# Performance work log

Hardware: AMD Instinct MI355X
Metric: run time of the kernel (lower is better)

## Reference

```python
import jax, jax.numpy as jnp
import numpy as np

N = 50000
E_RAND = 800000
IN0 = 128
HEADS = 4
C = 64  # per-head out channels
HC = HEADS * C  # 256, concat output width
SLOPE = 0.2
DIMS_IN = [IN0, HC, HC]


def _gat_layer(x, src, dst, W, att_src, att_dst, bias):
    # x: [N, F_in]; W: [F_in, H*C]; att_*: [H, C]; bias: [H*C]
    h = (x @ W).reshape(N, HEADS, C)                      # [N,H,C]
    a_src = jnp.einsum('nhc,hc->nh', h, att_src)          # [N,H]
    a_dst = jnp.einsum('nhc,hc->nh', h, att_dst)          # [N,H]
    e = jax.nn.leaky_relu(a_src[src] + a_dst[dst], SLOPE)  # [E,H]
    # segment softmax over incoming edges per destination node
    m = jax.ops.segment_max(e, dst, num_segments=N)       # [N,H]
    m = jnp.where(jnp.isfinite(m), m, 0.0)
    ex = jnp.exp(e - m[dst])                              # [E,H]
    denom = jax.ops.segment_sum(ex, dst, num_segments=N)  # [N,H]
    alpha = ex / (denom[dst] + 1e-16)                     # [E,H]
    msg = h[src] * alpha[:, :, None]                      # [E,H,C]
    out = jax.ops.segment_sum(msg, dst, num_segments=N)   # [N,H,C]
    return out.reshape(N, HC) + bias


def setup_inputs() -> dict:
    key = jax.random.key(0)
    ks = jax.random.split(key, 16)
    x = jax.random.normal(ks[0], (N, IN0), dtype=jnp.float32)
    src = jax.random.randint(ks[1], (E_RAND,), 0, N, dtype=jnp.int32)
    dst = jax.random.randint(ks[2], (E_RAND,), 0, N, dtype=jnp.int32)
    loops = jnp.arange(N, dtype=jnp.int32)  # PyG GATConv adds self-loops
    edge_index = jnp.stack([jnp.concatenate([src, loops]),
                            jnp.concatenate([dst, loops])])  # [2, E_RAND+N]
    inp = {'x': x, 'edge_index': edge_index}
    ki = 3
    for l, f_in in enumerate(DIMS_IN):
        s = 1.0 / np.sqrt(f_in)
        inp[f'W{l}'] = jax.random.uniform(ks[ki], (f_in, HC), jnp.float32, -s, s)
        inp[f'att_src{l}'] = jax.random.uniform(ks[ki + 1], (HEADS, C), jnp.float32, -s, s)
        inp[f'att_dst{l}'] = jax.random.uniform(ks[ki + 2], (HEADS, C), jnp.float32, -s, s)
        inp[f'bias{l}'] = jnp.zeros((HC,), jnp.float32)
        ki += 3
    return inp


def reference(x, edge_index, W0, att_src0, att_dst0, bias0,
              W1, att_src1, att_dst1, bias1,
              W2, att_src2, att_dst2, bias2):
    src, dst = edge_index[0], edge_index[1]
    params = [(W0, att_src0, att_dst0, bias0),
              (W1, att_src1, att_dst1, bias1),
              (W2, att_src2, att_dst2, bias2)]
    for W, a_s, a_d, b in params:
        x = jax.nn.relu(_gat_layer(x, src, dst, W, a_s, a_d, b))
    return x
```

## Files before the change

kernel.cpp:

```cpp
#include <hip/hip_runtime.h>
#include <hip/hip_fp16.h>
#include <math.h>

#define IN0    128
#define HEADS  4
#define CDIM   64
#define HC     256
#define SLOPE  0.2f
#define NPAD   50176
#define BK     32

typedef __attribute__((ext_vector_type(8))) _Float16 f16x8;
typedef __attribute__((ext_vector_type(4))) float f32x4;

__device__ __forceinline__ float h2f(ushort u) {
    __half h = *(const __half*)&u;
    return __half2float(h);
}
__device__ __forceinline__ ushort f2h(float f) {
    __half h = __float2half_rn(f);
    return *(ushort*)&h;
}


__device__ __forceinline__ void wconv_body(const float* __restrict__ W,
                                           ushort* __restrict__ Wc, int K, int b) {
    int tid = b * 256 + threadIdx.x;
    int n = tid & 255;
    int k = tid >> 8;
    if (k >= K) return;
    Wc[(size_t)(k >> 5) * (HC * BK) + n * BK + (k & 31)] = f2h(W[(size_t)k * HC + n]);
}

__global__ __launch_bounds__(256) void k_prep(
        const int* __restrict__ dst_rand, int E_rand, int* __restrict__ deg,
        const float* __restrict__ x0, ushort* __restrict__ Xc, int totalx,
        const float* __restrict__ W0, ushort* __restrict__ Wc0,
        const float* __restrict__ W1, ushort* __restrict__ Wc1,
        const float* __restrict__ W2, ushort* __restrict__ Wc2,
        int B0, int B1) {
    int b = blockIdx.x;
    if (b < B0) {
        int i = b * 256 + threadIdx.x;
        if (i < E_rand) atomicAdd(&deg[dst_rand[i]], 1);
        return;
    }
    b -= B0;
    if (b < B1) {
        int i = b * 256 + threadIdx.x;
        if (i < totalx) {
            int n = i >> 7, k = i & 127;
            Xc[(size_t)(k >> 5) * (NPAD * BK) + n * BK + (k & 31)] = f2h(x0[i]);
        }
        return;
    }
    b -= B1;
    if (b < 128) { wconv_body(W0, Wc0, 128, b); return; }
    b -= 128;
    if (b < 256) { wconv_body(W1, Wc1, 256, b); return; }
    b -= 256;
    wconv_body(W2, Wc2, 256, b);
}


__global__ __launch_bounds__(1024) void k_scan(const int* __restrict__ deg, int Nn,
                                               int* __restrict__ rowptr,
                                               int* __restrict__ cur) {
    __shared__ int smem[1024];
    int tid = threadIdx.x;
    int pre = 0;
    int limit = blockIdx.x * 1024;
    for (int i = tid; i < limit; i += 1024) pre += deg[i];
    smem[tid] = pre;
    __syncthreads();
    #pragma unroll
    for (int d = 512; d >= 1; d >>= 1) {
        if (tid < d) smem[tid] += smem[tid + d];
        __syncthreads();
    }
    int s_off = smem[0];
    __syncthreads();
    int i = blockIdx.x * 1024 + tid;
    int v = (i < Nn) ? deg[i] : 0;
    smem[tid] = v;
    __syncthreads();
    #pragma unroll
    for (int d = 1; d < 1024; d <<= 1) {
        int t = 0;
        if (tid >= d) t = smem[tid - d];
        __syncthreads();
        smem[tid] += t;
        __syncthreads();
    }
    if (i < Nn) {
        int e = s_off + smem[tid] - v;
        rowptr[i] = e;
        cur[i] = e;
    }
    if (blockIdx.x == gridDim.x - 1 && tid == 1023) rowptr[Nn] = s_off + smem[1023];
}

__global__ void k_scatter(const int* __restrict__ src, const int* __restrict__ dst, int E_rand,
                          int* __restrict__ cur, int* __restrict__ csr_src) {
    int i = blockIdx.x * blockDim.x + threadIdx.x;
    if (i < E_rand) {
        int d = dst[i];
        int p = atomicAdd(&cur[d], 1);
        csr_src[p] = src[i];
    }
}


template<int K>
__global__ __launch_bounds__(256) void k_gemm_att(const ushort* __restrict__ Xc,
                                                  const ushort* __restrict__ Wc,
                                                  const float* __restrict__ attS,
                                                  const float* __restrict__ attD,
                                                  ushort* __restrict__ H16out,
                                                  float* __restrict__ a_src_v,
                                                  float* __restrict__ a_dst_v,
                                                  int M) {
    int id    = blockIdx.x;
    int group = id >> 4;
    int sub   = id & 15;
    int row0  = (group * 8 + (sub & 7)) * 128;
    int colb  = sub >> 3;
    int col0  = colb * 128;

    int t    = threadIdx.x;
    int wave = t >> 6, lane = t & 63;
    int wm = wave & 1, wn = wave >> 1;
    int quad = lane >> 4, l16 = lane & 15;

    f32x4 acc[4][4];
    #pragma unroll
    for (int i = 0; i < 4; i++)
        #pragma unroll
        for (int j = 0; j < 4; j++) acc[i][j] = (f32x4){0.f, 0.f, 0.f, 0.f};

    constexpr int NK = K / BK;
    #pragma unroll
    for (int kc = 0; kc < NK; kc++) {
        f16x8 a[4], b[4];
        #pragma unroll
        for (int mt = 0; mt < 4; mt++) {
            size_t ga = (size_t)kc * (NPAD * BK)
                      + (size_t)(row0 + wm * 64 + mt * 16 + l16) * BK + quad * 8;
            a[mt] = *(const f16x8*)&Xc[ga];
        }
        #pragma unroll
        for (int nt = 0; nt < 4; nt++) {
            size_t gb = (size_t)kc * (HC * BK)
                      + (size_t)(col0 + wn * 64 + nt * 16 + l16) * BK + quad * 8;
            b[nt] = *(const f16x8*)&Wc[gb];
        }
        #pragma unroll
        for (int mt = 0; mt < 4; mt++)
            #pragma unroll
            for (int nt = 0; nt < 4; nt++)
                acc[mt][nt] = __builtin_amdgcn_mfma_f32_16x16x32_f16(a[mt], b[nt], acc[mt][nt], 0, 0, 0);
    }

    #pragma unroll
    for (int mt = 0; mt < 4; mt++) {
        #pragma unroll
        for (int r = 0; r < 4; r++) {
            int row = row0 + wm*64 + mt*16 + quad*4 + r;
            if (row >= M) continue;
            #pragma unroll
            for (int nt = 0; nt < 4; nt++) {
                size_t idx = (size_t)row * HC + col0 + wn*64 + nt*16 + l16;
                H16out[idx] = f2h(acc[mt][nt][r]);
            }
        }
    }

    int headw = colb * 2 + wn;
    float sS[4], sD[4];
    #pragma unroll
    for (int nt = 0; nt < 4; nt++) {
        sS[nt] = attS[headw * CDIM + nt*16 + l16];
        sD[nt] = attD[headw * CDIM + nt*16 + l16];
    }
    #pragma unroll
    for (int mt = 0; mt < 4; mt++) {
        #pragma unroll
        for (int r = 0; r < 4; r++) {
            float ps = 0.f, pd = 0.f;
            #pragma unroll
            for (int nt = 0; nt < 4; nt++) {
                float av = acc[mt][nt][r];
                ps += av * sS[nt];
                pd += av * sD[nt];
            }
            #pragma unroll
            for (int d = 1; d <= 8; d <<= 1) {
                ps += __shfl_xor(ps, d);
                pd += __shfl_xor(pd, d);
            }
            int row = row0 + wm*64 + mt*16 + quad*4 + r;
            if (l16 == 0 && row < M) {
                a_src_v[row * HEADS + headw] = ps;
                a_dst_v[row * HEADS + headw] = pd;
            }
        }
    }
}


__global__ __launch_bounds__(256) void k_aggregate(
        const ushort* __restrict__ H16,
        const float* __restrict__ a_src_v, const float* __restrict__ a_dst_v,
        const int* __restrict__ rowptr, const int* __restrict__ csr_src,
        const float* __restrict__ bias,
        float* __restrict__ out_f32,
        ushort* __restrict__ out_h16c,
        int Nn) {
    int wave = threadIdx.x >> 6;
    int lane = threadIdx.x & 63;
    int n = blockIdx.x * 4 + wave;
    if (n >= Nn) return;

    int e16 = lane >> 2;
    int hs  = lane & 3;
    int ha  = lane >> 4;
    int c4  = (lane & 15) * 4;

    int beg = rowptr[n], end = rowptr[n + 1];
    int deg = end - beg;
    float adst_s = a_dst_v[n * HEADS + hs];
    float es = a_src_v[n * HEADS + hs] + adst_s;
    es = (es > 0.f) ? es : SLOPE * es;
    float ex_self_s = __expf(es);

    float ssum = 0.f;
    float4 acc = make_float4(0.f, 0.f, 0.f, 0.f);
    const char* Hb = (const char*)H16 + (ha * CDIM + c4) * 2;

    for (int base = 0; base < deg; base += 16) {
        int cnt = min(16, deg - base);
        int s_l = 0; float ex_l = 0.f;
        if (e16 < cnt) {
            s_l = csr_src[beg + base + e16];
            float e = a_src_v[s_l * HEADS + hs] + adst_s;
            e = (e > 0.f) ? e : SLOPE * e;
            ex_l = __expf(e);
            ssum += ex_l;
        }
        int off_l = s_l * (HC * 2);
        int cnt4 = (cnt + 3) & ~3;
        for (int j = 0; j < cnt4; j += 4) {
            float a0 = __shfl(ex_l,  (j + 0) * 4 + ha);
            int   o0 = __shfl(off_l, (j + 0) * 4 + ha);
            float a1 = __shfl(ex_l,  (j + 1) * 4 + ha);
            int   o1 = __shfl(off_l, (j + 1) * 4 + ha);
            float a2 = __shfl(ex_l,  (j + 2) * 4 + ha);
            int   o2 = __shfl(off_l, (j + 2) * 4 + ha);
            float a3 = __shfl(ex_l,  (j + 3) * 4 + ha);
            int   o3 = __shfl(off_l, (j + 3) * 4 + ha);
            ushort4 u0 = *(const ushort4*)(Hb + o0);
            ushort4 u1 = *(const ushort4*)(Hb + o1);
            ushort4 u2 = *(const ushort4*)(Hb + o2);
            ushort4 u3 = *(const ushort4*)(Hb + o3);
            acc.x += a0 * h2f(u0.x); acc.y += a0 * h2f(u0.y);
            acc.z += a0 * h2f(u0.z); acc.w += a0 * h2f(u0.w);
            acc.x += a1 * h2f(u1.x); acc.y += a1 * h2f(u1.y);
            acc.z += a1 * h2f(u1.z); acc.w += a1 * h2f(u1.w);
            acc.x += a2 * h2f(u2.x); acc.y += a2 * h2f(u2.y);
            acc.z += a2 * h2f(u2.z); acc.w += a2 * h2f(u2.w);
            acc.x += a3 * h2f(u3.x); acc.y += a3 * h2f(u3.y);
            acc.z += a3 * h2f(u3.z); acc.w += a3 * h2f(u3.w);
        }
    }
    #pragma unroll
    for (int d = 4; d <= 32; d <<= 1) ssum += __shfl_xor(ssum, d);
    ssum += ex_self_s;
    float den_a = __shfl(ssum, ha);
    float exs_a = __shfl(ex_self_s, ha);

    ushort4 us = *(const ushort4*)((const char*)H16 + (size_t)n * (HC * 2) + (ha * CDIM + c4) * 2);
    float rden = 1.f / (den_a + 1e-16f);
    float4 b = *(const float4*)&bias[ha * CDIM + c4];
    float4 o;
    o.x = fmaxf((acc.x + exs_a * h2f(us.x)) * rden + b.x, 0.f);
    o.y = fmaxf((acc.y + exs_a * h2f(us.y)) * rden + b.y, 0.f);
    o.z = fmaxf((acc.z + exs_a * h2f(us.z)) * rden + b.z, 0.f);
    o.w = fmaxf((acc.w + exs_a * h2f(us.w)) * rden + b.w, 0.f);

    if (out_f32) {
        *(float4*)&out_f32[(size_t)n * HC + ha * CDIM + c4] = o;
    }
    if (out_h16c) {
        int ch = ha * CDIM + c4;
        size_t idx = (size_t)(ch >> 5) * (NPAD * BK) + (size_t)n * BK + (ch & 31);
        *(ushort4*)&out_h16c[idx] = make_ushort4(f2h(o.x), f2h(o.y), f2h(o.z), f2h(o.w));
    }
}


extern "C" void kernel_launch(void* const* d_in, const int* in_sizes, int n_in,
                              void* d_out, int out_size, void* d_ws, size_t ws_size,
                              hipStream_t stream) {
    const float* x0   = (const float*)d_in[0];
    const int*   eidx = (const int*)d_in[1];
    int Nn = in_sizes[0] / IN0;
    int E  = in_sizes[1] / 2;
    int E_rand = E - Nn;
    const int* srcp = eidx;
    const int* dstp = eidx + E;

    const float* Wl[3]    = {(const float*)d_in[2],  (const float*)d_in[6],  (const float*)d_in[10]};
    const float* attS[3]  = {(const float*)d_in[3],  (const float*)d_in[7],  (const float*)d_in[11]};
    const float* attD[3]  = {(const float*)d_in[4],  (const float*)d_in[8],  (const float*)d_in[12]};
    const float* biasl[3] = {(const float*)d_in[5],  (const float*)d_in[9],  (const float*)d_in[13]};
    int Kdims[3] = {IN0, HC, HC};

    char* p = (char*)d_ws;
    ushort* h16    = (ushort*)p; p += (size_t)NPAD * HC * sizeof(ushort);
    ushort* Xc     = (ushort*)p; p += (size_t)NPAD * HC * sizeof(ushort);
    float*  a_src_v= (float*)p;  p += (size_t)Nn * HEADS * sizeof(float);
    float*  a_dst_v= (float*)p;  p += (size_t)Nn * HEADS * sizeof(float);
    int*    rowptr = (int*)p;    p += (size_t)(Nn + 1) * sizeof(int);
    int*    deg    = (int*)p;    p += (size_t)Nn * sizeof(int);
    int*    cur    = (int*)p;    p += (size_t)Nn * sizeof(int);
    int*    csr_src= (int*)p;    p += (size_t)E_rand * sizeof(int);
    ushort* Wc[3];
    for (int l = 0; l < 3; l++) {
        Wc[l] = (ushort*)p; p += (size_t)HC * Kdims[l] * sizeof(ushort);
    }

    int NB = (Nn + 1023) / 1024;
    int B0 = (E_rand + 255) / 256;
    int B1 = (Nn * IN0 + 255) / 256;
    int Bprep = B0 + B1 + 128 + 256 + 256;

    hipMemsetAsync(deg, 0, (size_t)Nn * sizeof(int), stream);
    k_prep<<<Bprep, 256, 0, stream>>>(dstp, E_rand, deg,
                                      x0, Xc, Nn * IN0,
                                      Wl[0], Wc[0], Wl[1], Wc[1], Wl[2], Wc[2],
                                      B0, B1);
    k_scan<<<NB, 1024, 0, stream>>>(deg, Nn, rowptr, cur);
    k_scatter<<<(E_rand + 255) / 256, 256, 0, stream>>>(srcp, dstp, E_rand, cur, csr_src);

    dim3 g(784);
    dim3 ga((Nn + 3) / 4);
    for (int l = 0; l < 3; l++) {
        if (l == 0)
            k_gemm_att<128><<<g, 256, 0, stream>>>(Xc, Wc[l], attS[l], attD[l],
                                                   h16, a_src_v, a_dst_v, Nn);
        else
            k_gemm_att<256><<<g, 256, 0, stream>>>(Xc, Wc[l], attS[l], attD[l],
                                                   h16, a_src_v, a_dst_v, Nn);
        if (l < 2) {
            k_aggregate<<<ga, 256, 0, stream>>>(h16, a_src_v, a_dst_v, rowptr, csr_src,
                                                biasl[l], nullptr, Xc, Nn);
        } else {
            k_aggregate<<<ga, 256, 0, stream>>>(h16, a_src_v, a_dst_v, rowptr, csr_src,
                                                biasl[l], (float*)d_out, nullptr, Nn);
        }
    }
}
```

Measured before the change: 383.3 us.

## Store H in channel-sliced layout and split aggregation into 8 column slices

The GEMM now writes H in a 32-channel-sliced column-major-block layout and stores attention logits head-major. Aggregation launches 8 blocks per node group, each handling one 32-channel slice, so gathered rows are contiguous 64-byte chunks and blockIdx ordering keeps each slice's working set in cache. This trades more redundant softmax/index work (computed once per slice) for smaller, more cache-local gathers and more parallelism.

```diff
diff --git a/kernel.cpp b/kernel.cpp
--- a/kernel.cpp
+++ b/kernel.cpp
@@ -169,7 +169,8 @@
             if (row >= M) continue;
             #pragma unroll
             for (int nt = 0; nt < 4; nt++) {
-                size_t idx = (size_t)row * HC + col0 + wn*64 + nt*16 + l16;
+                int col = col0 + wn*64 + nt*16 + l16;
+                size_t idx = (size_t)(col >> 5) * (NPAD * 32) + (size_t)row * 32 + (col & 31);
                 H16out[idx] = f2h(acc[mt][nt][r]);
             }
         }
@@ -200,8 +201,8 @@
             }
             int row = row0 + wm*64 + mt*16 + quad*4 + r;
             if (l16 == 0 && row < M) {
-                a_src_v[row * HEADS + headw] = ps;
-                a_dst_v[row * HEADS + headw] = pd;
+                a_src_v[(size_t)headw * M + row] = ps;
+                a_dst_v[(size_t)headw * M + row] = pd;
             }
         }
     }
@@ -209,91 +210,84 @@
 
 
 __global__ __launch_bounds__(256) void k_aggregate(
-        const ushort* __restrict__ H16,
-        const float* __restrict__ a_src_v, const float* __restrict__ a_dst_v,
+        const ushort* __restrict__ Hc,
+        const float* __restrict__ a_srcP,
+        const float* __restrict__ a_dstP,
         const int* __restrict__ rowptr, const int* __restrict__ csr_src,
         const float* __restrict__ bias,
         float* __restrict__ out_f32,
         ushort* __restrict__ out_h16c,
         int Nn) {
-    int wave = threadIdx.x >> 6;
-    int lane = threadIdx.x & 63;
-    int n = blockIdx.x * 4 + wave;
+    int lane  = threadIdx.x & 63;
+    int slice = blockIdx.x & 7;
+    int n = (blockIdx.x >> 3) * 4 + (threadIdx.x >> 6);
     if (n >= Nn) return;
-
-    int e16 = lane >> 2;
-    int hs  = lane & 3;
-    int ha  = lane >> 4;
-    int c4  = (lane & 15) * 4;
+    int h  = slice >> 1;
+    int es = lane >> 3;
+    int c8 = lane & 7;
+
+    const char* Hs = (const char*)(Hc + (size_t)slice * (NPAD * 32));
+    const float* aS = a_srcP + (size_t)h * Nn;
 
     int beg = rowptr[n], end = rowptr[n + 1];
     int deg = end - beg;
-    float adst_s = a_dst_v[n * HEADS + hs];
-    float es = a_src_v[n * HEADS + hs] + adst_s;
-    es = (es > 0.f) ? es : SLOPE * es;
-    float ex_self_s = __expf(es);
+    float adst = a_dstP[(size_t)h * Nn + n];
+    float e_self = aS[n] + adst;
+    e_self = (e_self > 0.f) ? e_self : SLOPE * e_self;
+    float ex_self = __expf(e_self);
 
     float ssum = 0.f;
     float4 acc = make_float4(0.f, 0.f, 0.f, 0.f);
-    const char* Hb = (const char*)H16 + (ha * CDIM + c4) * 2;
-
-    for (int base = 0; base < deg; base += 16) {
-        int cnt = min(16, deg - base);
+
+    for (int base = 0; base < deg; base += 64) {
+        int cnt = min(64, deg - base);
         int s_l = 0; float ex_l = 0.f;
-        if (e16 < cnt) {
-            s_l = csr_src[beg + base + e16];
-            float e = a_src_v[s_l * HEADS + hs] + adst_s;
+        if (lane < cnt) {
+            s_l = csr_src[beg + base + lane];
+            float e = aS[s_l] + adst;
             e = (e > 0.f) ? e : SLOPE * e;
             ex_l = __expf(e);
             ssum += ex_l;
         }
-        int off_l = s_l * (HC * 2);
-        int cnt4 = (cnt + 3) & ~3;
-        for (int j = 0; j < cnt4; j += 4) {
-            float a0 = __shfl(ex_l,  (j + 0) * 4 + ha);
-            int   o0 = __shfl(off_l, (j + 0) * 4 + ha);
-            float a1 = __shfl(ex_l,  (j + 1) * 4 + ha);
-            int   o1 = __shfl(off_l, (j + 1) * 4 + ha);
-            float a2 = __shfl(ex_l,  (j + 2) * 4 + ha);
-            int   o2 = __shfl(off_l, (j + 2) * 4 + ha);
-            float a3 = __shfl(ex_l,  (j + 3) * 4 + ha);
-            int   o3 = __shfl(off_l, (j + 3) * 4 + ha);
-            ushort4 u0 = *(const ushort4*)(Hb + o0);
-            ushort4 u1 = *(const ushort4*)(Hb + o1);
-            ushort4 u2 = *(const ushort4*)(Hb + o2);
-            ushort4 u3 = *(const ushort4*)(Hb + o3);
-            acc.x += a0 * h2f(u0.x); acc.y += a0 * h2f(u0.y);
-            acc.z += a0 * h2f(u0.z); acc.w += a0 * h2f(u0.w);
-            acc.x += a1 * h2f(u1.x); acc.y += a1 * h2f(u1.y);
-            acc.z += a1 * h2f(u1.z); acc.w += a1 * h2f(u1.w);
-            acc.x += a2 * h2f(u2.x); acc.y += a2 * h2f(u2.y);
-            acc.z += a2 * h2f(u2.z); acc.w += a2 * h2f(u2.w);
-            acc.x += a3 * h2f(u3.x); acc.y += a3 * h2f(u3.y);
-            acc.z += a3 * h2f(u3.z); acc.w += a3 * h2f(u3.w);
-        }
-    }
-    #pragma unroll
-    for (int d = 4; d <= 32; d <<= 1) ssum += __shfl_xor(ssum, d);
-    ssum += ex_self_s;
-    float den_a = __shfl(ssum, ha);
-    float exs_a = __shfl(ex_self_s, ha);
-
-    ushort4 us = *(const ushort4*)((const char*)H16 + (size_t)n * (HC * 2) + (ha * CDIM + c4) * 2);
-    float rden = 1.f / (den_a + 1e-16f);
-    float4 b = *(const float4*)&bias[ha * CDIM + c4];
-    float4 o;
-    o.x = fmaxf((acc.x + exs_a * h2f(us.x)) * rden + b.x, 0.f);
-    o.y = fmaxf((acc.y + exs_a * h2f(us.y)) * rden + b.y, 0.f);
-    o.z = fmaxf((acc.z + exs_a * h2f(us.z)) * rden + b.z, 0.f);
-    o.w = fmaxf((acc.w + exs_a * h2f(us.w)) * rden + b.w, 0.f);
-
-    if (out_f32) {
-        *(float4*)&out_f32[(size_t)n * HC + ha * CDIM + c4] = o;
-    }
-    if (out_h16c) {
-        int ch = ha * CDIM + c4;
-        size_t idx = (size_t)(ch >> 5) * (NPAD * BK) + (size_t)n * BK + (ch & 31);
-        *(ushort4*)&out_h16c[idx] = make_ushort4(f2h(o.x), f2h(o.y), f2h(o.z), f2h(o.w));
+        int off_l = s_l * 64;
+        int cnt8 = (cnt + 7) & ~7;
+        for (int j = 0; j < cnt8; j += 8) {
+            float a = __shfl(ex_l,  j + es);
+            int   o = __shfl(off_l, j + es);
+            ushort4 u = *(const ushort4*)(Hs + o + c8 * 8);
+            acc.x += a * h2f(u.x);
+            acc.y += a * h2f(u.y);
+            acc.z += a * h2f(u.z);
+            acc.w += a * h2f(u.w);
+        }
+    }
+    #pragma unroll
+    for (int d = 1; d < 64; d <<= 1) ssum += __shfl_xor(ssum, d);
+    ssum += ex_self;
+    #pragma unroll
+    for (int d = 8; d <= 32; d <<= 1) {
+        acc.x += __shfl_xor(acc.x, d);
+        acc.y += __shfl_xor(acc.y, d);
+        acc.z += __shfl_xor(acc.z, d);
+        acc.w += __shfl_xor(acc.w, d);
+    }
+    float rden = 1.f / (ssum + 1e-16f);
+    ushort4 us = *(const ushort4*)(Hs + (size_t)n * 64 + c8 * 8);
+    int ch = slice * 32 + c8 * 4;
+    float4 b = *(const float4*)&bias[ch];
+    float4 o4;
+    o4.x = fmaxf((acc.x + ex_self * h2f(us.x)) * rden + b.x, 0.f);
+    o4.y = fmaxf((acc.y + ex_self * h2f(us.y)) * rden + b.y, 0.f);
+    o4.z = fmaxf((acc.z + ex_self * h2f(us.z)) * rden + b.z, 0.f);
+    o4.w = fmaxf((acc.w + ex_self * h2f(us.w)) * rden + b.w, 0.f);
+    if (es == 0) {
+        if (out_f32) {
+            *(float4*)&out_f32[(size_t)n * HC + ch] = o4;
+        }
+        if (out_h16c) {
+            size_t idx = (size_t)slice * (NPAD * 32) + (size_t)n * 32 + c8 * 4;
+            *(ushort4*)&out_h16c[idx] = make_ushort4(f2h(o4.x), f2h(o4.y), f2h(o4.z), f2h(o4.w));
+        }
     }
 }
 
@@ -343,7 +337,7 @@
     k_scatter<<<(E_rand + 255) / 256, 256, 0, stream>>>(srcp, dstp, E_rand, cur, csr_src);
 
     dim3 g(784);
-    dim3 ga((Nn + 3) / 4);
+    dim3 ga(8 * ((Nn + 3) / 4));
     for (int l = 0; l < 3; l++) {
         if (l == 0)
             k_gemm_att<128><<<g, 256, 0, stream>>>(Xc, Wc[l], attS[l], attD[l],
```

Result: slower. 633.6 us (+65.3%).

## Split aggregation across two blocks per node by head pairs

Applied to the files above, without the earlier changes.

The aggregate kernel now launches two blocks per group of four nodes. Each block handles two of the four heads (128 channels), so each wave processes two edges at a time in parallel half-waves and combines the two partial accumulators with a cross-half shuffle. This doubles the number of waves to raise memory-level parallelism and occupancy for the gather-heavy aggregation. In exchange, rowptr, csr_src and attention scores are read twice per node, more shuffles are needed, and half the lanes stay idle during the store.

```diff
diff --git a/kernel.cpp b/kernel.cpp
--- a/kernel.cpp
+++ b/kernel.cpp
@@ -210,90 +210,94 @@
 
 __global__ __launch_bounds__(256) void k_aggregate(
         const ushort* __restrict__ H16,
-        const float* __restrict__ a_src_v, const float* __restrict__ a_dst_v,
+        const float* __restrict__ a_src_v,
+        const float* __restrict__ a_dst_v,
         const int* __restrict__ rowptr, const int* __restrict__ csr_src,
         const float* __restrict__ bias,
         float* __restrict__ out_f32,
         ushort* __restrict__ out_h16c,
         int Nn) {
-    int wave = threadIdx.x >> 6;
-    int lane = threadIdx.x & 63;
-    int n = blockIdx.x * 4 + wave;
+    int wave  = threadIdx.x >> 6;
+    int lane  = threadIdx.x & 63;
+    int slice = blockIdx.x & 1;
+    int n = (blockIdx.x >> 1) * 4 + wave;
     if (n >= Nn) return;
 
-    int e16 = lane >> 2;
-    int hs  = lane & 3;
-    int ha  = lane >> 4;
+    int e32 = lane >> 1;
+    int hs2 = lane & 1;
+    int hgl = slice * 2 + hs2;
+    int e2  = lane >> 5;
+    int ha2 = (lane >> 4) & 1;
     int c4  = (lane & 15) * 4;
+    int chS = ha2 * CDIM + c4;
 
     int beg = rowptr[n], end = rowptr[n + 1];
     int deg = end - beg;
-    float adst_s = a_dst_v[n * HEADS + hs];
-    float es = a_src_v[n * HEADS + hs] + adst_s;
-    es = (es > 0.f) ? es : SLOPE * es;
+    float adst_s = a_dst_v[n * HEADS + hgl];
+    float es = a_src_v[n * HEADS + hgl] + adst_s;
+    es = fmaxf(es, SLOPE * es);
     float ex_self_s = __expf(es);
 
     float ssum = 0.f;
     float4 acc = make_float4(0.f, 0.f, 0.f, 0.f);
-    const char* Hb = (const char*)H16 + (ha * CDIM + c4) * 2;
-
-    for (int base = 0; base < deg; base += 16) {
-        int cnt = min(16, deg - base);
+    const char* Hb = (const char*)H16 + (size_t)(slice * 128 + chS) * 2;
+
+    for (int base = 0; base < deg; base += 32) {
+        int cnt = min(32, deg - base);
         int s_l = 0; float ex_l = 0.f;
-        if (e16 < cnt) {
-            s_l = csr_src[beg + base + e16];
-            float e = a_src_v[s_l * HEADS + hs] + adst_s;
-            e = (e > 0.f) ? e : SLOPE * e;
+        if (e32 < cnt) {
+            s_l = csr_src[beg + base + e32];
+            float e = a_src_v[s_l * HEADS + hgl] + adst_s;
+            e = fmaxf(e, SLOPE * e);
             ex_l = __expf(e);
             ssum += ex_l;
         }
         int off_l = s_l * (HC * 2);
         int cnt4 = (cnt + 3) & ~3;
         for (int j = 0; j < cnt4; j += 4) {
-            float a0 = __shfl(ex_l,  (j + 0) * 4 + ha);
-            int   o0 = __shfl(off_l, (j + 0) * 4 + ha);
-            float a1 = __shfl(ex_l,  (j + 1) * 4 + ha);
-            int   o1 = __shfl(off_l, (j + 1) * 4 + ha);
-            float a2 = __shfl(ex_l,  (j + 2) * 4 + ha);
-            int   o2 = __shfl(off_l, (j + 2) * 4 + ha);
-            float a3 = __shfl(ex_l,  (j + 3) * 4 + ha);
-            int   o3 = __shfl(off_l, (j + 3) * 4 + ha);
+            int sl0 = ((j + e2) << 1) | ha2;
+            int sl1 = ((j + 2 + e2) << 1) | ha2;
+            float a0 = __shfl(ex_l,  sl0);
+            int   o0 = __shfl(off_l, sl0);
+            float a1 = __shfl(ex_l,  sl1);
+            int   o1 = __shfl(off_l, sl1);
             ushort4 u0 = *(const ushort4*)(Hb + o0);
             ushort4 u1 = *(const ushort4*)(Hb + o1);
-            ushort4 u2 = *(const ushort4*)(Hb + o2);
-            ushort4 u3 = *(const ushort4*)(Hb + o3);
             acc.x += a0 * h2f(u0.x); acc.y += a0 * h2f(u0.y);
             acc.z += a0 * h2f(u0.z); acc.w += a0 * h2f(u0.w);
             acc.x += a1 * h2f(u1.x); acc.y += a1 * h2f(u1.y);
             acc.z += a1 * h2f(u1.z); acc.w += a1 * h2f(u1.w);
-            acc.x += a2 * h2f(u2.x); acc.y += a2 * h2f(u2.y);
-            acc.z += a2 * h2f(u2.z); acc.w += a2 * h2f(u2.w);
-            acc.x += a3 * h2f(u3.x); acc.y += a3 * h2f(u3.y);
-            acc.z += a3 * h2f(u3.z); acc.w += a3 * h2f(u3.w);
-        }
-    }
-    #pragma unroll
-    for (int d = 4; d <= 32; d <<= 1) ssum += __shfl_xor(ssum, d);
+        }
+    }
+    #pragma unroll
+    for (int d = 2; d <= 32; d <<= 1) ssum += __shfl_xor(ssum, d);
     ssum += ex_self_s;
-    float den_a = __shfl(ssum, ha);
-    float exs_a = __shfl(ex_self_s, ha);
-
-    ushort4 us = *(const ushort4*)((const char*)H16 + (size_t)n * (HC * 2) + (ha * CDIM + c4) * 2);
+    acc.x += __shfl_xor(acc.x, 32);
+    acc.y += __shfl_xor(acc.y, 32);
+    acc.z += __shfl_xor(acc.z, 32);
+    acc.w += __shfl_xor(acc.w, 32);
+    float den_a = __shfl(ssum, ha2);
+    float exs_a = __shfl(ex_self_s, ha2);
+
+    ushort4 us = *(const ushort4*)((const char*)H16 + (size_t)n * (HC * 2)
+                                   + (size_t)(slice * 128 + chS) * 2);
     float rden = 1.f / (den_a + 1e-16f);
-    float4 b = *(const float4*)&bias[ha * CDIM + c4];
+    int ch = slice * 128 + chS;
+    float4 b = *(const float4*)&bias[ch];
     float4 o;
     o.x = fmaxf((acc.x + exs_a * h2f(us.x)) * rden + b.x, 0.f);
     o.y = fmaxf((acc.y + exs_a * h2f(us.y)) * rden + b.y, 0.f);
     o.z = fmaxf((acc.z + exs_a * h2f(us.z)) * rden + b.z, 0.f);
     o.w = fmaxf((acc.w + exs_a * h2f(us.w)) * rden + b.w, 0.f);
 
-    if (out_f32) {
-        *(float4*)&out_f32[(size_t)n * HC + ha * CDIM + c4] = o;
-    }
-    if (out_h16c) {
-        int ch = ha * CDIM + c4;
-        size_t idx = (size_t)(ch >> 5) * (NPAD * BK) + (size_t)n * BK + (ch & 31);
-        *(ushort4*)&out_h16c[idx] = make_ushort4(f2h(o.x), f2h(o.y), f2h(o.z), f2h(o.w));
+    if (e2 == 0) {
+        if (out_f32) {
+            *(float4*)&out_f32[(size_t)n * HC + ch] = o;
+        }
+        if (out_h16c) {
+            size_t idx = (size_t)(ch >> 5) * (NPAD * BK) + (size_t)n * BK + (ch & 31);
+            *(ushort4*)&out_h16c[idx] = make_ushort4(f2h(o.x), f2h(o.y), f2h(o.z), f2h(o.w));
+        }
     }
 }
 
@@ -343,7 +347,7 @@
     k_scatter<<<(E_rand + 255) / 256, 256, 0, stream>>>(srcp, dstp, E_rand, cur, csr_src);
 
     dim3 g(784);
-    dim3 ga((Nn + 3) / 4);
+    dim3 ga(2 * ((Nn + 3) / 4));
     for (int l = 0; l < 3; l++) {
         if (l == 0)
             k_gemm_att<128><<<g, 256, 0, stream>>>(Xc, Wc[l], attS[l], attD[l],
```

Result: slower. 394.2 us (+2.8%).
